# Kernel tuning notes

Measured on AMD Instinct MI355X. Metric: run time of the kernel, lower is better.

Reference implementation:

```python
import jax, jax.numpy as jnp
import numpy as np

B, N, T, H, F = 2, 1024, 12, 64, 1

def _diffuse(x, a):
    # x: (B,C,V), a: (B,W,V)  ->  (B,C,W)   (einsum 'ncvl,nwv->ncwl' with l=1)
    return jnp.einsum('bcv,bwv->bcw', x, a)

def _sconv(x, supports, order, include_self, W, b):
    feats = [x] if include_self else []
    for a in supports:
        x1 = _diffuse(x, a)
        feats.append(x1)
        for _ in range(order - 1):
            x1 = _diffuse(x1, a)
            feats.append(x1)
    z = jnp.concatenate(feats, axis=1)
    return jnp.einsum('bcn,oc->bon', z, W) + b[None, :, None]

def _lin(x, W, b):
    # Conv1d/Conv2d with kernel 1 == channel-wise linear
    return jnp.einsum('bcn,oc->bon', x, W) + b[None, :, None]

def setup_inputs():
    key = jax.random.key(0)
    ks = jax.random.split(key, 12)
    x = jax.random.normal(ks[0], (B, F, N, T), jnp.float32)
    mask = jax.random.randint(ks[1], (B, F, N, T), 0, 2, jnp.int32)
    adj = jax.random.uniform(ks[2], (2, B, N, N), jnp.float32)
    adj = adj / (adj.sum(-1, keepdims=True) + 1e-8)  # compute_support row-normalization
    cin_gate = 5 * (2 * F + H)  # (order*support_len+1)*(d_in+num_units) = 5*66
    s = 0.1
    Wr = s * jax.random.normal(ks[3], (H, cin_gate)); br = jnp.zeros((H,), jnp.float32)
    Wu = s * jax.random.normal(ks[4], (H, cin_gate)); bu = jnp.zeros((H,), jnp.float32)
    Wc = s * jax.random.normal(ks[5], (H, cin_gate)); bc = jnp.zeros((H,), jnp.float32)
    Wfs = s * jax.random.normal(ks[6], (F, H)); bfs = jnp.zeros((F,), jnp.float32)
    Wdin = s * jax.random.normal(ks[7], (H, 2 * F + H)); bdin = jnp.zeros((H,), jnp.float32)
    Wgc = s * jax.random.normal(ks[8], (H, 2 * H)); bgc = jnp.zeros((H,), jnp.float32)
    Wlout = s * jax.random.normal(ks[9], (H, 2 * H)); blout = jnp.zeros((H,), jnp.float32)
    Wro = s * jax.random.normal(ks[10], (F, 2 * H)); bro = jnp.zeros((F,), jnp.float32)
    prelu_a = 0.25 * jnp.ones((1,), jnp.float32)
    return dict(x=x, mask=mask, adj=adj, Wr=Wr, br=br, Wu=Wu, bu=bu, Wc=Wc, bc=bc,
                Wfs=Wfs, bfs=bfs, Wdin=Wdin, bdin=bdin, Wgc=Wgc, bgc=bgc,
                Wlout=Wlout, blout=blout, Wro=Wro, bro=bro, prelu_a=prelu_a)

def _gril(x, mask, adj, Wr, br, Wu, bu, Wc, bc, Wfs, bfs, Wdin, bdin,
          Wgc, bgc, Wlout, blout, Wro, bro, prelu_a):
    supports = [adj[0], adj[1]]
    h0 = jnp.zeros((x.shape[0], H, x.shape[2]), x.dtype)

    def step(h, inp):
        x_s, m_s = inp                  # (B,F,N), (B,F,N) int
        m_f = m_s.astype(x_s.dtype)
        m_b = m_s.astype(bool)
        # first stage prediction from hidden state
        xs1 = _lin(h, Wfs, bfs)
        x1 = jnp.where(m_b, x_s, xs1)
        # spatial decoder (order=1, no attention)
        x_in = _lin(jnp.concatenate([x1, m_f, h], axis=1), Wdin, bdin)
        out = _sconv(x_in, supports, 1, False, Wgc, bgc)
        out = _lin(jnp.concatenate([out, h], axis=1), Wlout, blout)
        out = jnp.where(out >= 0, out, prelu_a * out)   # PReLU
        repr_s = jnp.concatenate([out, h], axis=1)      # (B,2H,N)
        xs2 = _lin(repr_s, Wro, bro)
        x2 = jnp.where(m_b, x1, xs2)
        # GCGRU cell update (order=2 diffusion per gate)
        inp_c = jnp.concatenate([x2, m_f], axis=1)
        xh = jnp.concatenate([inp_c, h], axis=1)
        r = jax.nn.sigmoid(_sconv(xh, supports, 2, True, Wr, br))
        u = jax.nn.sigmoid(_sconv(xh, supports, 2, True, Wu, bu))
        xc = jnp.concatenate([inp_c, r * h], axis=1)
        c = jnp.tanh(_sconv(xc, supports, 2, True, Wc, bc))
        h_new = u * h + (1.0 - u) * c
        return h_new, (xs2, xs1, repr_s)

    xs = jnp.moveaxis(x, -1, 0)     # (T,B,F,N)
    ms = jnp.moveaxis(mask, -1, 0)
    _, (imps, preds, reprs) = jax.lax.scan(step, h0, (xs, ms))
    imputations = jnp.moveaxis(imps, 0, -1)       # (B,F,N,T)
    predictions = jnp.moveaxis(preds, 0, -1)      # (B,F,N,T)
    representations = jnp.moveaxis(reprs, 0, -1)  # (B,2H,N,T)
    return imputations, predictions, representations

def reference(x, mask, adj, Wr, br, Wu, bu, Wc, bc, Wfs, bfs, Wdin, bdin,
              Wgc, bgc, Wlout, blout, Wro, bro, prelu_a):
    return _gril(x, mask, adj, Wr, br, Wu, bu, Wc, bc, Wfs, bfs, Wdin, bdin,
                 Wgc, bgc, Wlout, blout, Wro, bro, prelu_a)
```

## Files before the change

kernel.cpp:

```cpp
#include <hip/hip_runtime.h>
#include <hip/hip_bf16.h>
#include <cstddef>

#define NN 1024
#define BB 2
#define TT 12
#define ZS 352

typedef __attribute__((ext_vector_type(8))) short short8;
typedef __attribute__((ext_vector_type(4))) short short4v;
typedef __attribute__((ext_vector_type(4))) float f32x4;
typedef __hip_bfloat16 bf16;

__device__ __forceinline__ float sigmoidf_(float v) { return 1.0f / (1.0f + expf(-v)); }
__device__ __forceinline__ short bf16s(float f) { bf16 h = __float2bfloat16(f); return *reinterpret_cast<short*>(&h); }

__device__ __forceinline__ float mapcol(const float* src, int c) {
    if (c < 64) return src[2 + c];
    if (c == 64) return src[0];
    if (c == 65) return src[1];
    if (c < 68 || c >= 340) return 0.f;
    const int d = c - 68, bk = d / 68, off = d % 68;
    if (off < 64) return src[66 + bk * 66 + 2 + off];
    if (off == 64) return src[66 + bk * 66];
    if (off == 65) return src[66 + bk * 66 + 1];
    return 0.f;
}

__global__ __launch_bounds__(256) void k_prep(
    const float* __restrict__ Wgc, const float* __restrict__ bgc,
    const float* __restrict__ Wdin, const float* __restrict__ bdin,
    const float* __restrict__ Wlout, const float* __restrict__ blout,
    const float* __restrict__ Wfs,
    const float* __restrict__ Wr, const float* __restrict__ Wu, const float* __restrict__ Wc,
    float* __restrict__ Wcomb, float* __restrict__ bcomb, float* __restrict__ blout2,
    bf16* __restrict__ Wpre, bf16* __restrict__ Wrub, bf16* __restrict__ Wcb,
    bf16* __restrict__ Wlb)
{
    const int idx = blockIdx.x * 256 + threadIdx.x;
    if (idx < 8448) {
        const int o = idx / 66, k = idx % 66;
        const float* g = Wgc + (size_t)(o & 63) * 128 + (o >> 6) * 64;
        float a = 0.f;
#pragma unroll 8
        for (int c = 0; c < 64; ++c) a += g[c] * Wdin[c * 66 + k];
        Wcomb[idx] = a;
    } else if (idx < 8576) {
        const int o = idx - 8448;
        const float* g = Wgc + (size_t)(o & 63) * 128 + (o >> 6) * 64;
        float a = 0.f;
#pragma unroll 8
        for (int c = 0; c < 64; ++c) a += g[c] * bdin[c];
        bcomb[o] = a;
    } else if (idx < 8640) {
        const int oc = idx - 8576;
        float a = blout[oc];
#pragma unroll 8
        for (int j = 0; j < 64; ++j) a += Wlout[(size_t)oc * 128 + j] * bgc[j];
        blout2[oc] = a;
    } else if (idx < 17856) {
        const int j = idx - 8640, r = j >> 6, k = j & 63;
        float v = 0.f;
        if (r == 0) v = Wfs[k];
        else if (r <= 128) {
            const int o = r - 1;
            const float* g = Wgc + (size_t)(o & 63) * 128 + (o >> 6) * 64;
#pragma unroll 8
            for (int c = 0; c < 64; ++c) v += g[c] * Wdin[c * 66 + 2 + k];
        }
        Wpre[j] = __float2bfloat16(v);
    } else if (idx < 62912) {
        const int j = idx - 17856, r = j / 352, c = j % 352;
        const float* src = (r < 64) ? (Wr + (size_t)r * 330) : (Wu + (size_t)(r - 64) * 330);
        Wrub[j] = __float2bfloat16(mapcol(src, c));
    } else if (idx < 85440) {
        const int j = idx - 62912, r = j / 352, c = j % 352;
        Wcb[j] = __float2bfloat16(mapcol(Wc + (size_t)r * 330, c));
    } else if (idx < 93632) {
        const int j = idx - 85440;
        Wlb[j] = __float2bfloat16(Wlout[j]);
    }
}

__global__ __launch_bounds__(256) void k_cvtT(const float* __restrict__ adj,
                                              bf16* __restrict__ adjb, bf16* __restrict__ adjtb)
{
    const int sb = blockIdx.z;
    const int r0 = blockIdx.y * 64, c0 = blockIdx.x * 64;
    const float* A = adj + ((size_t)sb << 20);
    __shared__ short tile[64][72];
    const int tr = threadIdx.x >> 4, tc = (threadIdx.x & 15) * 4;
#pragma unroll
    for (int i = 0; i < 4; ++i) {
        const int r = tr + i * 16;
        float4 v = *reinterpret_cast<const float4*>(&A[(size_t)(r0 + r) * NN + c0 + tc]);
        short4v o = { bf16s(v.x), bf16s(v.y), bf16s(v.z), bf16s(v.w) };
        *reinterpret_cast<short4v*>(&adjb[((size_t)sb << 20) + (size_t)(r0 + r) * NN + c0 + tc]) = o;
        tile[r][tc + 0] = o.x; tile[r][tc + 1] = o.y; tile[r][tc + 2] = o.z; tile[r][tc + 3] = o.w;
    }
    __syncthreads();
#pragma unroll
    for (int i = 0; i < 4; ++i) {
        const int v = tr + i * 16;
        short4v o = { tile[tc + 0][v], tile[tc + 1][v], tile[tc + 2][v], tile[tc + 3][v] };
        *reinterpret_cast<short4v*>(&adjtb[((size_t)sb << 20) + (size_t)(c0 + v) * NN + r0 + tc]) = o;
    }
}

__global__ __launch_bounds__(256) void k_a2(const bf16* __restrict__ adjb,
                                            const bf16* __restrict__ adjtb,
                                            bf16* __restrict__ adj2b)
{
    const int sb = blockIdx.z;
    const int wave = threadIdx.x >> 6, lane = threadIdx.x & 63;
    const int lr = lane & 15, lq = lane >> 4;
    const int v0 = blockIdx.x * 128 + wave * 32;
    const int w0 = blockIdx.y * 64;
    const bf16* AT = adjtb + ((size_t)sb << 20) + (size_t)(v0 + lr) * NN + lq * 8;
    const bf16* Ar = adjb + ((size_t)sb << 20) + (size_t)(w0 + lr) * NN + lq * 8;
    f32x4 acc[4][2];
#pragma unroll
    for (int m = 0; m < 4; ++m)
#pragma unroll
        for (int nb = 0; nb < 2; ++nb) acc[m][nb] = (f32x4){0.f, 0.f, 0.f, 0.f};

    short8 bfr[2], af[4];
#pragma unroll
    for (int nb = 0; nb < 2; ++nb) bfr[nb] = *reinterpret_cast<const short8*>(AT + (size_t)nb * 16 * NN);
#pragma unroll
    for (int m = 0; m < 4; ++m) af[m] = *reinterpret_cast<const short8*>(Ar + (size_t)m * 16 * NN);

#pragma unroll 4
    for (int k0 = 0; k0 < NN; k0 += 32) {
        short8 bfr_n[2], af_n[4];
        const int kn = k0 + 32;
        if (kn < NN) {
#pragma unroll
            for (int nb = 0; nb < 2; ++nb)
                bfr_n[nb] = *reinterpret_cast<const short8*>(AT + (size_t)nb * 16 * NN + kn);
#pragma unroll
            for (int m = 0; m < 4; ++m)
                af_n[m] = *reinterpret_cast<const short8*>(Ar + (size_t)m * 16 * NN + kn);
        }
#pragma unroll
        for (int m = 0; m < 4; ++m)
#pragma unroll
            for (int nb = 0; nb < 2; ++nb)
                acc[m][nb] = __builtin_amdgcn_mfma_f32_16x16x32_bf16(af[m], bfr[nb], acc[m][nb], 0, 0, 0);
        if (kn < NN) {
#pragma unroll
            for (int nb = 0; nb < 2; ++nb) bfr[nb] = bfr_n[nb];
#pragma unroll
            for (int m = 0; m < 4; ++m) af[m] = af_n[m];
        }
    }
    bf16* D = adj2b + ((size_t)sb << 20);
#pragma unroll
    for (int m = 0; m < 4; ++m)
#pragma unroll
        for (int nb = 0; nb < 2; ++nb)
#pragma unroll
            for (int q = 0; q < 4; ++q)
                D[(size_t)(w0 + m * 16 + lq * 4 + q) * NN + v0 + nb * 16 + lr] = __float2bfloat16(acc[m][nb][q]);
}

__global__ __launch_bounds__(64) void k_pre(
    const bf16* __restrict__ Wpre, const bf16* __restrict__ zT,
    const float* __restrict__ Wcomb, const float* __restrict__ bcomb,
    const float* __restrict__ bfsp,
    const float* __restrict__ x, const int* __restrict__ mask,
    bf16* __restrict__ yb, float* __restrict__ pred, int t)
{
    const int lane = threadIdx.x & 63, lr = lane & 15, lq = lane >> 4;
    const int p = blockIdx.x * 16 + lr;
    const bf16* B = zT + (size_t)p * ZS;
    f32x4 acc[9];
#pragma unroll
    for (int m = 0; m < 9; ++m) acc[m] = (f32x4){0.f, 0.f, 0.f, 0.f};
#pragma unroll
    for (int ks = 0; ks < 2; ++ks) {
        short8 bfr = *reinterpret_cast<const short8*>(B + ks * 32 + lq * 8);
#pragma unroll
        for (int m = 0; m < 9; ++m) {
            short8 af = *reinterpret_cast<const short8*>(Wpre + (size_t)(m * 16 + lr) * 64 + ks * 32 + lq * 8);
            acc[m] = __builtin_amdgcn_mfma_f32_16x16x32_bf16(af, bfr, acc[m], 0, 0, 0);
        }
    }
    const int b = p >> 10, n = p & (NN - 1);
    const size_t xi = (size_t)p * TT + t;
    const float xs1v = acc[0][0] + bfsp[0];
    const float xs1 = __shfl(xs1v, lr);
    const int mi = mask[xi];
    const float mf = (float)mi;
    const float x1 = mi ? x[xi] : xs1;
    if (lq == 0) pred[xi] = xs1;
#pragma unroll
    for (int m = 0; m < 9; ++m)
#pragma unroll
        for (int q = 0; q < 4; ++q) {
            const int o = m * 16 + lq * 4 + q - 1;
            if (o >= 0 && o < 128) {
                const float val = acc[m][q] + Wcomb[o * 66] * x1 + Wcomb[o * 66 + 1] * mf + bcomb[o];
                yb[(size_t)(b * 128 + o) * NN + n] = __float2bfloat16(val);
            }
        }
}

__global__ __launch_bounds__(256) void k_difA(
    const bf16* __restrict__ adjb, const bf16* __restrict__ adj2b,
    const bf16* __restrict__ yb, const bf16* __restrict__ zbi,
    const bf16* __restrict__ Wlb, const float* __restrict__ blout2,
    const float* __restrict__ prelu_a, const float* __restrict__ Wro,
    const float* __restrict__ bro, const float* __restrict__ x,
    const int* __restrict__ mask, const float* __restrict__ hTf,
    float* __restrict__ imp, float* __restrict__ repr,
    bf16* __restrict__ zb, bf16* __restrict__ zcb,
    bf16* __restrict__ zT, bf16* __restrict__ zcT, int t)
{
    const int wave = threadIdx.x >> 6, lane = threadIdx.x & 63;
    const int lr = lane & 15, lq = lane >> 4;
    const int n0 = blockIdx.x * 32;

    __shared__ f32x4 red[3][2][2][4][64];
    __shared__ short gh[32][136];
    __shared__ float hf[32][68];
    __shared__ float lo_sm[32][68];

    if (blockIdx.y >= 2) {
        const int i = blockIdx.y - 2;
        const int b = i & 1, s = (i >> 1) & 1, ord = i >> 2;
        const int sb = s * 2 + b;
        const bf16* M = (ord ? adj2b : adjb) + ((size_t)sb << 20);
        const bf16* A = M + (size_t)(n0 + lr) * NN + lq * 8;
        const bf16* Xp = zbi + ((size_t)(b * 66 + lr)) * NN + lq * 8;
        f32x4 acc[2][4];
#pragma unroll
        for (int nt = 0; nt < 2; ++nt)
#pragma unroll
            for (int m = 0; m < 4; ++m) acc[nt][m] = (f32x4){0.f, 0.f, 0.f, 0.f};
        const int vbeg = wave * 256;
#pragma unroll 2
        for (int it = 0; it < 8; ++it) {
            const int v0 = vbeg + it * 32;
            short8 bfr[2], af[4];
#pragma unroll
            for (int nt = 0; nt < 2; ++nt)
                bfr[nt] = *reinterpret_cast<const short8*>(A + (size_t)nt * 16 * NN + v0);
#pragma unroll
            for (int m = 0; m < 4; ++m)
                af[m] = *reinterpret_cast<const short8*>(Xp + (size_t)m * 16 * NN + v0);
#pragma unroll
            for (int nt = 0; nt < 2; ++nt)
#pragma unroll
                for (int m = 0; m < 4; ++m)
                    acc[nt][m] = __builtin_amdgcn_mfma_f32_16x16x32_bf16(af[m], bfr[nt], acc[nt][m], 0, 0, 0);
        }
        if (wave > 0) {
#pragma unroll
            for (int nt = 0; nt < 2; ++nt)
#pragma unroll
                for (int m = 0; m < 4; ++m) red[wave - 1][0][nt][m][lane] = acc[nt][m];
        }
        __syncthreads();
        if (wave == 0) {
#pragma unroll
            for (int nt = 0; nt < 2; ++nt) {
#pragma unroll
                for (int m = 0; m < 4; ++m)
                    acc[nt][m] += red[0][0][nt][m][lane] + red[1][0][nt][m][lane] + red[2][0][nt][m][lane];
                const int p = b * NN + n0 + nt * 16 + lr;
                bf16* dst = zT + (size_t)p * ZS + 68 + (s * 2 + ord) * 68;
#pragma unroll
                for (int m = 0; m < 4; ++m) {
                    short4v o = { bf16s(acc[nt][m][0]), bf16s(acc[nt][m][1]),
                                  bf16s(acc[nt][m][2]), bf16s(acc[nt][m][3]) };
                    *reinterpret_cast<short4v*>(dst + m * 16 + lq * 4) = o;
                }
            }
        }
        return;
    }

    const int b = blockIdx.y;
    f32x4 acc[2][2][4];
#pragma unroll
    for (int s = 0; s < 2; ++s)
#pragma unroll
        for (int nt = 0; nt < 2; ++nt)
#pragma unroll
            for (int m = 0; m < 4; ++m) acc[s][nt][m] = (f32x4){0.f, 0.f, 0.f, 0.f};
    {
        const int vbeg = wave * 256;
#pragma unroll 2
        for (int it = 0; it < 8; ++it) {
            const int v0 = vbeg + it * 32;
            short8 bfr[2][2], af[2][4];
#pragma unroll
            for (int s = 0; s < 2; ++s) {
                const bf16* M = adjb + ((size_t)(s * 2 + b) << 20);
#pragma unroll
                for (int nt = 0; nt < 2; ++nt)
                    bfr[s][nt] = *reinterpret_cast<const short8*>(M + (size_t)(n0 + nt * 16 + lr) * NN + v0 + lq * 8);
#pragma unroll
                for (int m = 0; m < 4; ++m)
                    af[s][m] = *reinterpret_cast<const short8*>(yb + (size_t)(b * 128 + s * 64 + m * 16 + lr) * NN + v0 + lq * 8);
            }
#pragma unroll
            for (int s = 0; s < 2; ++s)
#pragma unroll
                for (int nt = 0; nt < 2; ++nt)
#pragma unroll
                    for (int m = 0; m < 4; ++m)
                        acc[s][nt][m] = __builtin_amdgcn_mfma_f32_16x16x32_bf16(af[s][m], bfr[s][nt], acc[s][nt][m], 0, 0, 0);
        }
    }
    if (wave > 0) {
#pragma unroll
        for (int s = 0; s < 2; ++s)
#pragma unroll
            for (int nt = 0; nt < 2; ++nt)
#pragma unroll
                for (int m = 0; m < 4; ++m) red[wave - 1][s][nt][m][lane] = acc[s][nt][m];
    }
    if (wave == 1 || wave == 2) {
        const int nb = (wave - 1) * 16;
        for (int i = lane; i < 1024; i += 64) {
            const int node = nb + (i >> 6), oc = i & 63;
            const float hv = hTf[(size_t)(b * NN + n0 + node) * 64 + oc];
            hf[node][oc] = hv;
            gh[node][64 + oc] = bf16s(hv);
            repr[(((size_t)b * 128 + 64 + oc) * NN + (n0 + node)) * TT + t] = hv;
        }
    }
    __syncthreads();
    if (wave == 0) {
#pragma unroll
        for (int nt = 0; nt < 2; ++nt) {
#pragma unroll
            for (int m = 0; m < 4; ++m) {
                f32x4 g = acc[0][nt][m] + acc[1][nt][m];
#pragma unroll
                for (int w = 0; w < 3; ++w) g += red[w][0][nt][m][lane] + red[w][1][nt][m][lane];
                const int node = nt * 16 + lr;
#pragma unroll
                for (int q = 0; q < 4; ++q) gh[node][m * 16 + lq * 4 + q] = bf16s(g[q]);
            }
        }
    }
    __syncthreads();
    {
        f32x4 dacc[2];
#pragma unroll
        for (int nt = 0; nt < 2; ++nt) dacc[nt] = (f32x4){0.f, 0.f, 0.f, 0.f};
#pragma unroll
        for (int ks = 0; ks < 4; ++ks) {
            short8 af = *reinterpret_cast<const short8*>(Wlb + (size_t)(wave * 16 + lr) * 128 + ks * 32 + lq * 8);
#pragma unroll
            for (int nt = 0; nt < 2; ++nt) {
                short8 bfr = *reinterpret_cast<const short8*>(&gh[nt * 16 + lr][ks * 32 + lq * 8]);
                dacc[nt] = __builtin_amdgcn_mfma_f32_16x16x32_bf16(af, bfr, dacc[nt], 0, 0, 0);
            }
        }
        const float pa = prelu_a[0];
#pragma unroll
        for (int nt = 0; nt < 2; ++nt) {
            const int node = nt * 16 + lr;
#pragma unroll
            for (int q = 0; q < 4; ++q) {
                const int oc = wave * 16 + lq * 4 + q;
                float v = dacc[nt][q] + blout2[oc];
                v = (v >= 0.f) ? v : pa * v;
                repr[(((size_t)b * 128 + oc) * NN + (n0 + node)) * TT + t] = v;
                lo_sm[node][oc] = v;
            }
        }
    }
    __syncthreads();
    {
        const int node = threadIdx.x >> 3, sub = threadIdx.x & 7;
        float s = 0.f;
#pragma unroll
        for (int j = sub * 8; j < sub * 8 + 8; ++j)
            s += Wro[j] * lo_sm[node][j] + Wro[64 + j] * hf[node][j];
        s += __shfl_xor(s, 1); s += __shfl_xor(s, 2); s += __shfl_xor(s, 4);
        if (sub == 0) {
            const float xs2 = s + bro[0];
            const int n = n0 + node;
            const int p = b * NN + n;
            const size_t xi = (size_t)p * TT + t;
            imp[xi] = xs2;
            const int mi = mask[xi];
            const float x2 = mi ? x[xi] : xs2;
            const bf16 x2b = __float2bfloat16(x2);
            const bf16 mb = __float2bfloat16((float)mi);
            zb[((size_t)b * 66 + 64) * NN + n] = x2b;
            zb[((size_t)b * 66 + 65) * NN + n] = mb;
            zT[(size_t)p * ZS + 64] = x2b; zT[(size_t)p * ZS + 65] = mb;
            zcT[(size_t)p * ZS + 64] = x2b; zcT[(size_t)p * ZS + 65] = mb;
        }
    }
}

__global__ __launch_bounds__(256) void k_difN(
    const bf16* __restrict__ adjb, const bf16* __restrict__ adj2b,
    const bf16* __restrict__ zcb, bf16* __restrict__ zcT)
{
    const int i = blockIdx.y;
    const int b = i & 1, s = (i >> 1) & 1, ord = i >> 2;
    const int wave = threadIdx.x >> 6, lane = threadIdx.x & 63;
    const int lr = lane & 15, lq = lane >> 4;
    const int n0 = blockIdx.x * 32;
    const int sb = s * 2 + b;
    const bf16* M = (ord ? adj2b : adjb) + ((size_t)sb << 20);
    const bf16* A = M + (size_t)(n0 + lr) * NN + lq * 8;
    const bf16* Xp = zcb + ((size_t)(b * 66 + lr)) * NN + lq * 8;

    f32x4 acc[2][4];
#pragma unroll
    for (int nt = 0; nt < 2; ++nt)
#pragma unroll
        for (int m = 0; m < 4; ++m) acc[nt][m] = (f32x4){0.f, 0.f, 0.f, 0.f};
    const int vbeg = wave * 256;

    short8 bfr[2], af[4];
#pragma unroll
    for (int nt = 0; nt < 2; ++nt)
        bfr[nt] = *reinterpret_cast<const short8*>(A + (size_t)nt * 16 * NN + vbeg);
#pragma unroll
    for (int m = 0; m < 4; ++m)
        af[m] = *reinterpret_cast<const short8*>(Xp + (size_t)m * 16 * NN + vbeg);

#pragma unroll 2
    for (int it = 0; it < 8; ++it) {
        const int vn = vbeg + it * 32 + 32;
        short8 bfr_n[2], af_n[4];
        if (it < 7) {
#pragma unroll
            for (int nt = 0; nt < 2; ++nt)
                bfr_n[nt] = *reinterpret_cast<const short8*>(A + (size_t)nt * 16 * NN + vn);
#pragma unroll
            for (int m = 0; m < 4; ++m)
                af_n[m] = *reinterpret_cast<const short8*>(Xp + (size_t)m * 16 * NN + vn);
        }
#pragma unroll
        for (int nt = 0; nt < 2; ++nt)
#pragma unroll
            for (int m = 0; m < 4; ++m)
                acc[nt][m] = __builtin_amdgcn_mfma_f32_16x16x32_bf16(af[m], bfr[nt], acc[nt][m], 0, 0, 0);
        if (it < 7) {
#pragma unroll
            for (int nt = 0; nt < 2; ++nt) bfr[nt] = bfr_n[nt];
#pragma unroll
            for (int m = 0; m < 4; ++m) af[m] = af_n[m];
        }
    }
    __shared__ f32x4 red[3][2][4][64];
    if (wave > 0) {
#pragma unroll
        for (int nt = 0; nt < 2; ++nt)
#pragma unroll
            for (int m = 0; m < 4; ++m) red[wave - 1][nt][m][lane] = acc[nt][m];
    }
    __syncthreads();
    if (wave == 0) {
#pragma unroll
        for (int nt = 0; nt < 2; ++nt) {
#pragma unroll
            for (int m = 0; m < 4; ++m)
                acc[nt][m] += red[0][nt][m][lane] + red[1][nt][m][lane] + red[2][nt][m][lane];
            const int p = b * NN + n0 + nt * 16 + lr;
            bf16* dst = zcT + (size_t)p * ZS + 68 + (s * 2 + ord) * 68;
#pragma unroll
            for (int m = 0; m < 4; ++m) {
                short4v o = { bf16s(acc[nt][m][0]), bf16s(acc[nt][m][1]),
                              bf16s(acc[nt][m][2]), bf16s(acc[nt][m][3]) };
                *reinterpret_cast<short4v*>(dst + m * 16 + lq * 4) = o;
            }
        }
    }
}

__global__ __launch_bounds__(256) void k_dif2(
    const bf16* __restrict__ adjb, const bf16* __restrict__ adj2b,
    const bf16* __restrict__ zb, bf16* __restrict__ zT, bf16* __restrict__ zcT)
{
    const int i = blockIdx.y;
    const int b = i & 1, s = (i >> 1) & 1, ord = i >> 2;
    const int sb = s * 2 + b;
    const int wave = threadIdx.x >> 6, lane = threadIdx.x & 63;
    const int lr = lane & 15, lq = lane >> 4;
    const int n0 = blockIdx.x * 16;
    const bf16* M = (ord ? adj2b : adjb) + ((size_t)sb << 20);
    const bf16* A = M + (size_t)(n0 + lr) * NN + lq * 8;
    const bf16* Xp = zb + ((size_t)(b * 66 + 64) + lr) * NN + lq * 8;

    f32x4 acc = (f32x4){0.f, 0.f, 0.f, 0.f};
    const short8 zsh = {0, 0, 0, 0, 0, 0, 0, 0};
    const int vbeg = wave * 256;
#pragma unroll 4
    for (int i2 = 0; i2 < 8; ++i2) {
        const int v0 = vbeg + i2 * 32;
        short8 bfr = *reinterpret_cast<const short8*>(A + v0);
        short8 af = (lr < 2) ? *reinterpret_cast<const short8*>(Xp + v0) : zsh;
        acc = __builtin_amdgcn_mfma_f32_16x16x32_bf16(af, bfr, acc, 0, 0, 0);
    }
    __shared__ f32x4 red2[3][64];
    if (wave > 0) red2[wave - 1][lane] = acc;
    __syncthreads();
    if (wave == 0 && lq == 0) {
        acc += red2[0][lane] + red2[1][lane] + red2[2][lane];
        const int p = b * NN + n0 + lr;
        const size_t off = (size_t)p * ZS + 68 + (s * 2 + ord) * 68 + 64;
#pragma unroll
        for (int q = 0; q < 2; ++q) {
            const bf16 v = __float2bfloat16(acc[q]);
            zT[off + q] = v; zcT[off + q] = v;
        }
    }
}

__global__ __launch_bounds__(128) void k_gates(
    const bf16* __restrict__ Wrub, const bf16* __restrict__ zT,
    const float* __restrict__ br, const float* __restrict__ bu,
    const float* __restrict__ hTf,
    float* __restrict__ uT, bf16* __restrict__ zcb, bf16* __restrict__ zcT)
{
    const int wave = threadIdx.x >> 6, lane = threadIdx.x & 63;
    const int lr = lane & 15, lq = lane >> 4;
    const int p = blockIdx.x * 16 + lr;
    const bf16* B = zT + (size_t)p * ZS;
    const bf16* WA = Wrub + (size_t)wave * 64 * ZS;
    f32x4 acc[4];
#pragma unroll
    for (int m = 0; m < 4; ++m) acc[m] = (f32x4){0.f, 0.f, 0.f, 0.f};
#pragma unroll 2
    for (int ks = 0; ks < 11; ++ks) {
        short8 bfr = *reinterpret_cast<const short8*>(B + ks * 32 + lq * 8);
#pragma unroll
        for (int m = 0; m < 4; ++m) {
            short8 af = *reinterpret_cast<const short8*>(WA + (size_t)(m * 16 + lr) * ZS + ks * 32 + lq * 8);
            acc[m] = __builtin_amdgcn_mfma_f32_16x16x32_bf16(af, bfr, acc[m], 0, 0, 0);
        }
    }
    const int b = p >> 10, n = p & (NN - 1);
    if (wave == 0) {
#pragma unroll
        for (int m = 0; m < 4; ++m) {
            short4v rq;
#pragma unroll
            for (int q = 0; q < 4; ++q) {
                const int oc = m * 16 + lq * 4 + q;
                const float rv = sigmoidf_(acc[m][q] + br[oc]);
                const float rh = rv * hTf[(size_t)p * 64 + oc];
                rq[q] = bf16s(rh);
                zcb[((size_t)b * 66 + oc) * NN + n] = __float2bfloat16(rh);
            }
            *reinterpret_cast<short4v*>(&zcT[(size_t)p * ZS + m * 16 + lq * 4]) = rq;
        }
    } else {
#pragma unroll
        for (int m = 0; m < 4; ++m) {
            f32x4 uq;
#pragma unroll
            for (int q = 0; q < 4; ++q) {
                const int oc = m * 16 + lq * 4 + q;
                uq[q] = sigmoidf_(acc[m][q] + bu[oc]);
            }
            *reinterpret_cast<f32x4*>(&uT[(size_t)p * 64 + m * 16 + lq * 4]) = uq;
        }
    }
}

__global__ __launch_bounds__(128) void k_cellpre(
    const bf16* __restrict__ Wcb, const bf16* __restrict__ zcT,
    const float* __restrict__ bc, const float* __restrict__ uT,
    float* __restrict__ hTf, bf16* __restrict__ zT, bf16* __restrict__ zb,
    const bf16* __restrict__ Wpre, const float* __restrict__ Wcomb,
    const float* __restrict__ bcomb, const float* __restrict__ bfsp,
    const float* __restrict__ x, const int* __restrict__ mask,
    bf16* __restrict__ yb, float* __restrict__ pred, int tn)
{
    const int wave = threadIdx.x >> 6, lane = threadIdx.x & 63;
    const int lr = lane & 15, lq = lane >> 4;
    const int p = blockIdx.x * 16 + lr;
    const int b = p >> 10, n = p & (NN - 1);
    __shared__ short hsm[16][72];
    __shared__ float xs1s[16];

    {
        const bf16* B = zcT + (size_t)p * ZS;
        f32x4 acc[2];
#pragma unroll
        for (int mm = 0; mm < 2; ++mm) acc[mm] = (f32x4){0.f, 0.f, 0.f, 0.f};
#pragma unroll 2
        for (int ks = 0; ks < 11; ++ks) {
            short8 bfr = *reinterpret_cast<const short8*>(B + ks * 32 + lq * 8);
#pragma unroll
            for (int mm = 0; mm < 2; ++mm) {
                const int m = wave * 2 + mm;
                short8 af = *reinterpret_cast<const short8*>(Wcb + (size_t)(m * 16 + lr) * ZS + ks * 32 + lq * 8);
                acc[mm] = __builtin_amdgcn_mfma_f32_16x16x32_bf16(af, bfr, acc[mm], 0, 0, 0);
            }
        }
#pragma unroll
        for (int mm = 0; mm < 2; ++mm) {
            const int m = wave * 2 + mm;
            f32x4 hq;
            short4v hb;
#pragma unroll
            for (int q = 0; q < 4; ++q) {
                const int oc = m * 16 + lq * 4 + q;
                const float cv = tanhf(acc[mm][q] + bc[oc]);
                const float uv = uT[(size_t)p * 64 + oc];
                const float ho = hTf[(size_t)p * 64 + oc];
                const float hn = uv * ho + (1.f - uv) * cv;
                hq[q] = hn;
                hb[q] = bf16s(hn);
                zb[((size_t)b * 66 + oc) * NN + n] = __float2bfloat16(hn);
            }
            *reinterpret_cast<f32x4*>(&hTf[(size_t)p * 64 + m * 16 + lq * 4]) = hq;
            *reinterpret_cast<short4v*>(&zT[(size_t)p * ZS + m * 16 + lq * 4]) = hb;
            *reinterpret_cast<short4v*>(&hsm[lr][m * 16 + lq * 4]) = hb;
        }
    }
    __syncthreads();

    {
        const int MB = wave ? 4 : 5;
        f32x4 acc[5];
#pragma unroll
        for (int m = 0; m < 5; ++m) acc[m] = (f32x4){0.f, 0.f, 0.f, 0.f};
#pragma unroll
        for (int ks = 0; ks < 2; ++ks) {
            short8 bfr = *reinterpret_cast<const short8*>(&hsm[lr][ks * 32 + lq * 8]);
#pragma unroll
            for (int m = 0; m < 5; ++m) {
                if (m < MB) {
                    const int mm = wave ? 5 + m : m;
                    short8 af = *reinterpret_cast<const short8*>(Wpre + (size_t)(mm * 16 + lr) * 64 + ks * 32 + lq * 8);
                    acc[m] = __builtin_amdgcn_mfma_f32_16x16x32_bf16(af, bfr, acc[m], 0, 0, 0);
                }
            }
        }
        if (wave == 0 && lq == 0) xs1s[lr] = acc[0][0] + bfsp[0];
        __syncthreads();
        const float xs1 = xs1s[lr];
        const size_t xi = (size_t)p * TT + tn;
        const int mi = mask[xi];
        const float mf = (float)mi;
        const float x1 = mi ? x[xi] : xs1;
        if (wave == 0 && lq == 0) pred[xi] = xs1;
#pragma unroll
        for (int m = 0; m < 5; ++m) {
            if (m < MB) {
                const int mm = wave ? 5 + m : m;
#pragma unroll
                for (int q = 0; q < 4; ++q) {
                    const int o = mm * 16 + lq * 4 + q - 1;
                    if (o >= 0 && o < 128) {
                        const float val = acc[m][q] + Wcomb[o * 66] * x1 + Wcomb[o * 66 + 1] * mf + bcomb[o];
                        yb[(size_t)(b * 128 + o) * NN + n] = __float2bfloat16(val);
                    }
                }
            }
        }
    }
}

extern "C" void kernel_launch(void* const* d_in, const int* in_sizes, int n_in,
                              void* d_out, int out_size, void* d_ws, size_t ws_size,
                              hipStream_t stream)
{
    const float* x     = (const float*)d_in[0];
    const int*   mask  = (const int*)  d_in[1];
    const float* adj   = (const float*)d_in[2];
    const float* Wr    = (const float*)d_in[3];
    const float* br    = (const float*)d_in[4];
    const float* Wu    = (const float*)d_in[5];
    const float* bu    = (const float*)d_in[6];
    const float* Wc    = (const float*)d_in[7];
    const float* bc    = (const float*)d_in[8];
    const float* Wfs   = (const float*)d_in[9];
    const float* bfs   = (const float*)d_in[10];
    const float* Wdin  = (const float*)d_in[11];
    const float* bdin  = (const float*)d_in[12];
    const float* Wgc   = (const float*)d_in[13];
    const float* bgc   = (const float*)d_in[14];
    const float* Wlout = (const float*)d_in[15];
    const float* blout = (const float*)d_in[16];
    const float* Wro   = (const float*)d_in[17];
    const float* bro   = (const float*)d_in[18];
    const float* pa    = (const float*)d_in[19];

    float* ws = (float*)d_ws;
    float* Wcomb  = ws + 0;
    float* bcomb  = ws + 8448;
    float* blout2 = ws + 8576;
    float* uT     = ws + 272832;
    float* hTf    = ws + 403904;
    bf16* bfp   = (bf16*)(ws + 534976);
    bf16* zb    = bfp + 0;
    bf16* zcb   = bfp + 135168;
    bf16* zT    = bfp + 270336;
    bf16* zcT   = bfp + 991232;
    bf16* adjb  = bfp + 1712128;
    bf16* adjtb = bfp + 5906432;
    bf16* adj2b = bfp + 10100736;
    bf16* yb    = bfp + 14295040;
    bf16* Wpre  = bfp + 14557184;
    bf16* Wrub  = bfp + 14566400;
    bf16* Wcb   = bfp + 14611456;
    bf16* Wlb   = bfp + 14633984;

    float* imp  = (float*)d_out;
    float* pred = imp + (size_t)BB * NN * TT;
    float* repr = imp + (size_t)2 * BB * NN * TT;

    hipMemsetAsync(hTf, 0, 131072 * 4 + (size_t)1712128 * 2, stream);
    hipLaunchKernelGGL(k_prep, dim3(366), dim3(256), 0, stream,
                       Wgc, bgc, Wdin, bdin, Wlout, blout, Wfs, Wr, Wu, Wc,
                       Wcomb, bcomb, blout2, Wpre, Wrub, Wcb, Wlb);
    hipLaunchKernelGGL(k_cvtT, dim3(16, 16, 4), dim3(256), 0, stream, adj, adjb, adjtb);
    hipLaunchKernelGGL(k_a2, dim3(8, 16, 4), dim3(256), 0, stream, adjb, adjtb, adj2b);

    hipLaunchKernelGGL(k_pre, dim3(128), dim3(64), 0, stream,
                       Wpre, zT, Wcomb, bcomb, bfs, x, mask, yb, pred, 0);

    for (int t = 0; t < TT; ++t) {
        const int ny = (t > 0 && t < TT - 1) ? 10 : 2;
        hipLaunchKernelGGL(k_difA, dim3(32, ny), dim3(256), 0, stream,
                           adjb, adj2b, yb, zb, Wlb, blout2, pa, Wro, bro, x, mask,
                           hTf, imp, repr, zb, zcb, zT, zcT, t);
        if (t < TT - 1) {
            hipLaunchKernelGGL(k_dif2, dim3(64, 8), dim3(256), 0, stream,
                               adjb, adj2b, zb, zT, zcT);
            hipLaunchKernelGGL(k_gates, dim3(128), dim3(128), 0, stream,
                               Wrub, zT, br, bu, hTf, uT, zcb, zcT);
            if (t > 0) {
                hipLaunchKernelGGL(k_difN, dim3(32, 8), dim3(256), 0, stream,
                                   adjb, adj2b, zcb, zcT);
            }
            hipLaunchKernelGGL(k_cellpre, dim3(128), dim3(128), 0, stream,
                               Wcb, zcT, bc, uT, hTf, zT, zb,
                               Wpre, Wcomb, bcomb, bfs, x, mask, yb, pred, t + 1);
        }
    }
}
```

Baseline: 695.5 us.

## Fuse mask-channel diffusion into gates kernel with rank-8 correction

```diff
diff --git a/kernel.cpp b/kernel.cpp
--- a/kernel.cpp
+++ b/kernel.cpp
@@ -26,6 +26,15 @@
     if (off == 65) return src[66 + bk * 66 + 1];
     return 0.f;
 }
+__device__ __forceinline__ float mapcolz(const float* src, int c) {
+    if (c < 64) return src[2 + c];
+    if (c == 64) return src[0];
+    if (c == 65) return src[1];
+    if (c < 68 || c >= 340) return 0.f;
+    const int d = c - 68, bk = d / 68, off = d % 68;
+    if (off < 64) return src[66 + bk * 66 + 2 + off];
+    return 0.f;
+}
 
 __global__ __launch_bounds__(256) void k_prep(
     const float* __restrict__ Wgc, const float* __restrict__ bgc,
@@ -35,7 +44,7 @@
     const float* __restrict__ Wr, const float* __restrict__ Wu, const float* __restrict__ Wc,
     float* __restrict__ Wcomb, float* __restrict__ bcomb, float* __restrict__ blout2,
     bf16* __restrict__ Wpre, bf16* __restrict__ Wrub, bf16* __restrict__ Wcb,
-    bf16* __restrict__ Wlb)
+    bf16* __restrict__ Wlb, float* __restrict__ Wrux)
 {
     const int idx = blockIdx.x * 256 + threadIdx.x;
     if (idx < 8448) {
@@ -72,13 +81,17 @@
     } else if (idx < 62912) {
         const int j = idx - 17856, r = j / 352, c = j % 352;
         const float* src = (r < 64) ? (Wr + (size_t)r * 330) : (Wu + (size_t)(r - 64) * 330);
-        Wrub[j] = __float2bfloat16(mapcol(src, c));
+        Wrub[j] = __float2bfloat16(mapcolz(src, c));
     } else if (idx < 85440) {
         const int j = idx - 62912, r = j / 352, c = j % 352;
         Wcb[j] = __float2bfloat16(mapcol(Wc + (size_t)r * 330, c));
     } else if (idx < 93632) {
         const int j = idx - 85440;
         Wlb[j] = __float2bfloat16(Wlout[j]);
+    } else if (idx < 94656) {
+        const int j2 = idx - 93632, r = j2 >> 3, j = j2 & 7;
+        const float* src = (r < 64) ? (Wr + (size_t)r * 330) : (Wu + (size_t)(r - 64) * 330);
+        Wrux[j2] = src[66 + (j >> 1) * 66 + (j & 1)];
     }
 }
 
@@ -111,11 +124,14 @@
                                             const bf16* __restrict__ adjtb,
                                             bf16* __restrict__ adj2b)
 {
-    const int sb = blockIdx.z;
+    const int L = blockIdx.x;
+    const int xv = L >> 6;
+    const int yz = L & 63;
+    const int w0 = (yz & 15) * 64;
+    const int sb = yz >> 4;
     const int wave = threadIdx.x >> 6, lane = threadIdx.x & 63;
     const int lr = lane & 15, lq = lane >> 4;
-    const int v0 = blockIdx.x * 128 + wave * 32;
-    const int w0 = blockIdx.y * 64;
+    const int v0 = xv * 128 + wave * 32;
     const bf16* AT = adjtb + ((size_t)sb << 20) + (size_t)(v0 + lr) * NN + lq * 8;
     const bf16* Ar = adjb + ((size_t)sb << 20) + (size_t)(w0 + lr) * NN + lq * 8;
     f32x4 acc[4][2];
@@ -123,36 +139,20 @@
     for (int m = 0; m < 4; ++m)
 #pragma unroll
         for (int nb = 0; nb < 2; ++nb) acc[m][nb] = (f32x4){0.f, 0.f, 0.f, 0.f};
-
-    short8 bfr[2], af[4];
-#pragma unroll
-    for (int nb = 0; nb < 2; ++nb) bfr[nb] = *reinterpret_cast<const short8*>(AT + (size_t)nb * 16 * NN);
-#pragma unroll
-    for (int m = 0; m < 4; ++m) af[m] = *reinterpret_cast<const short8*>(Ar + (size_t)m * 16 * NN);
-
 #pragma unroll 4
     for (int k0 = 0; k0 < NN; k0 += 32) {
-        short8 bfr_n[2], af_n[4];
-        const int kn = k0 + 32;
-        if (kn < NN) {
-#pragma unroll
-            for (int nb = 0; nb < 2; ++nb)
-                bfr_n[nb] = *reinterpret_cast<const short8*>(AT + (size_t)nb * 16 * NN + kn);
-#pragma unroll
-            for (int m = 0; m < 4; ++m)
-                af_n[m] = *reinterpret_cast<const short8*>(Ar + (size_t)m * 16 * NN + kn);
-        }
+        short8 bfr[2], af[4];
+#pragma unroll
+        for (int nb = 0; nb < 2; ++nb)
+            bfr[nb] = *reinterpret_cast<const short8*>(AT + (size_t)nb * 16 * NN + k0);
+#pragma unroll
+        for (int m = 0; m < 4; ++m)
+            af[m] = *reinterpret_cast<const short8*>(Ar + (size_t)m * 16 * NN + k0);
 #pragma unroll
         for (int m = 0; m < 4; ++m)
 #pragma unroll
             for (int nb = 0; nb < 2; ++nb)
                 acc[m][nb] = __builtin_amdgcn_mfma_f32_16x16x32_bf16(af[m], bfr[nb], acc[m][nb], 0, 0, 0);
-        if (kn < NN) {
-#pragma unroll
-            for (int nb = 0; nb < 2; ++nb) bfr[nb] = bfr_n[nb];
-#pragma unroll
-            for (int m = 0; m < 4; ++m) af[m] = af_n[m];
-        }
     }
     bf16* D = adj2b + ((size_t)sb << 20);
 #pragma unroll
@@ -480,93 +480,103 @@
     }
 }
 
-__global__ __launch_bounds__(256) void k_dif2(
-    const bf16* __restrict__ adjb, const bf16* __restrict__ adj2b,
-    const bf16* __restrict__ zb, bf16* __restrict__ zT, bf16* __restrict__ zcT)
-{
-    const int i = blockIdx.y;
-    const int b = i & 1, s = (i >> 1) & 1, ord = i >> 2;
-    const int sb = s * 2 + b;
-    const int wave = threadIdx.x >> 6, lane = threadIdx.x & 63;
-    const int lr = lane & 15, lq = lane >> 4;
-    const int n0 = blockIdx.x * 16;
-    const bf16* M = (ord ? adj2b : adjb) + ((size_t)sb << 20);
-    const bf16* A = M + (size_t)(n0 + lr) * NN + lq * 8;
-    const bf16* Xp = zb + ((size_t)(b * 66 + 64) + lr) * NN + lq * 8;
-
-    f32x4 acc = (f32x4){0.f, 0.f, 0.f, 0.f};
-    const short8 zsh = {0, 0, 0, 0, 0, 0, 0, 0};
-    const int vbeg = wave * 256;
-#pragma unroll 4
-    for (int i2 = 0; i2 < 8; ++i2) {
-        const int v0 = vbeg + i2 * 32;
-        short8 bfr = *reinterpret_cast<const short8*>(A + v0);
-        short8 af = (lr < 2) ? *reinterpret_cast<const short8*>(Xp + v0) : zsh;
-        acc = __builtin_amdgcn_mfma_f32_16x16x32_bf16(af, bfr, acc, 0, 0, 0);
-    }
-    __shared__ f32x4 red2[3][64];
-    if (wave > 0) red2[wave - 1][lane] = acc;
-    __syncthreads();
-    if (wave == 0 && lq == 0) {
-        acc += red2[0][lane] + red2[1][lane] + red2[2][lane];
-        const int p = b * NN + n0 + lr;
-        const size_t off = (size_t)p * ZS + 68 + (s * 2 + ord) * 68 + 64;
-#pragma unroll
-        for (int q = 0; q < 2; ++q) {
-            const bf16 v = __float2bfloat16(acc[q]);
-            zT[off + q] = v; zcT[off + q] = v;
-        }
-    }
-}
-
-__global__ __launch_bounds__(128) void k_gates(
+__global__ __launch_bounds__(512) void k_gates(
     const bf16* __restrict__ Wrub, const bf16* __restrict__ zT,
     const float* __restrict__ br, const float* __restrict__ bu,
     const float* __restrict__ hTf,
+    const bf16* __restrict__ adjb, const bf16* __restrict__ adj2b,
+    const bf16* __restrict__ zb, const float* __restrict__ Wrux,
     float* __restrict__ uT, bf16* __restrict__ zcb, bf16* __restrict__ zcT)
 {
     const int wave = threadIdx.x >> 6, lane = threadIdx.x & 63;
     const int lr = lane & 15, lq = lane >> 4;
     const int p = blockIdx.x * 16 + lr;
-    const bf16* B = zT + (size_t)p * ZS;
-    const bf16* WA = Wrub + (size_t)wave * 64 * ZS;
-    f32x4 acc[4];
-#pragma unroll
-    for (int m = 0; m < 4; ++m) acc[m] = (f32x4){0.f, 0.f, 0.f, 0.f};
+    const int b = blockIdx.x >> 6;
+    const int n0 = (blockIdx.x & 63) * 16;
+    const int n = p & (NN - 1);
+    __shared__ float xds[8][16];
+    __shared__ float wxs[128][8];
+
+    f32x4 acc[2];
+    acc[0] = (f32x4){0.f, 0.f, 0.f, 0.f};
+    acc[1] = (f32x4){0.f, 0.f, 0.f, 0.f};
+
+    if (wave < 4) {
+        const int ti = wave * 64 + lane;
+        reinterpret_cast<float4*>(&wxs[0][0])[ti] = reinterpret_cast<const float4*>(Wrux)[ti];
+        const bf16* B = zT + (size_t)p * ZS;
 #pragma unroll 2
-    for (int ks = 0; ks < 11; ++ks) {
-        short8 bfr = *reinterpret_cast<const short8*>(B + ks * 32 + lq * 8);
-#pragma unroll
-        for (int m = 0; m < 4; ++m) {
-            short8 af = *reinterpret_cast<const short8*>(WA + (size_t)(m * 16 + lr) * ZS + ks * 32 + lq * 8);
-            acc[m] = __builtin_amdgcn_mfma_f32_16x16x32_bf16(af, bfr, acc[m], 0, 0, 0);
-        }
-    }
-    const int b = p >> 10, n = p & (NN - 1);
-    if (wave == 0) {
-#pragma unroll
-        for (int m = 0; m < 4; ++m) {
-            short4v rq;
-#pragma unroll
-            for (int q = 0; q < 4; ++q) {
-                const int oc = m * 16 + lq * 4 + q;
-                const float rv = sigmoidf_(acc[m][q] + br[oc]);
-                const float rh = rv * hTf[(size_t)p * 64 + oc];
-                rq[q] = bf16s(rh);
-                zcb[((size_t)b * 66 + oc) * NN + n] = __float2bfloat16(rh);
-            }
-            *reinterpret_cast<short4v*>(&zcT[(size_t)p * ZS + m * 16 + lq * 4]) = rq;
+        for (int ks = 0; ks < 11; ++ks) {
+            short8 bfr = *reinterpret_cast<const short8*>(B + ks * 32 + lq * 8);
+#pragma unroll
+            for (int mm = 0; mm < 2; ++mm) {
+                short8 af = *reinterpret_cast<const short8*>(
+                    Wrub + (size_t)(wave * 32 + mm * 16 + lr) * ZS + ks * 32 + lq * 8);
+                acc[mm] = __builtin_amdgcn_mfma_f32_16x16x32_bf16(af, bfr, acc[mm], 0, 0, 0);
+            }
         }
     } else {
-#pragma unroll
-        for (int m = 0; m < 4; ++m) {
-            f32x4 uq;
-#pragma unroll
-            for (int q = 0; q < 4; ++q) {
-                const int oc = m * 16 + lq * 4 + q;
-                uq[q] = sigmoidf_(acc[m][q] + bu[oc]);
-            }
-            *reinterpret_cast<f32x4*>(&uT[(size_t)p * 64 + m * 16 + lq * 4]) = uq;
+        const int bk = wave - 4;
+        const int s = bk >> 1, ord = bk & 1;
+        const bf16* Mp = (ord ? adj2b : adjb) + ((size_t)(s * 2 + b) << 20)
+                         + (size_t)(n0 + lr) * NN + lq * 8;
+        const bf16* Xp = zb + (size_t)(b * 66 + 64 + lr) * NN + lq * 8;
+        const short8 zsh = {0, 0, 0, 0, 0, 0, 0, 0};
+        f32x4 a = (f32x4){0.f, 0.f, 0.f, 0.f};
+        short8 afv = (lr < 2) ? *reinterpret_cast<const short8*>(Xp) : zsh;
+        short8 mv = *reinterpret_cast<const short8*>(Mp);
+#pragma unroll 4
+        for (int it = 0; it < 32; ++it) {
+            short8 af_n, m_n;
+            if (it < 31) {
+                af_n = (lr < 2) ? *reinterpret_cast<const short8*>(Xp + (it + 1) * 32) : zsh;
+                m_n = *reinterpret_cast<const short8*>(Mp + (it + 1) * 32);
+            }
+            a = __builtin_amdgcn_mfma_f32_16x16x32_bf16(afv, mv, a, 0, 0, 0);
+            if (it < 31) { afv = af_n; mv = m_n; }
+        }
+        if (lq == 0) {
+            xds[bk * 2 + 0][lr] = a[0];
+            xds[bk * 2 + 1][lr] = a[1];
+            bf16* dst = zcT + (size_t)p * ZS + 68 + bk * 68 + 64;
+            dst[0] = __float2bfloat16(a[0]);
+            dst[1] = __float2bfloat16(a[1]);
+        }
+    }
+    __syncthreads();
+
+    if (wave < 4) {
+        if (wave < 2) {
+#pragma unroll
+            for (int mm = 0; mm < 2; ++mm) {
+                short4v rq;
+#pragma unroll
+                for (int q = 0; q < 4; ++q) {
+                    const int oc = wave * 32 + mm * 16 + lq * 4 + q;
+                    float corr = 0.f;
+#pragma unroll
+                    for (int j = 0; j < 8; ++j) corr += wxs[oc][j] * xds[j][lr];
+                    const float rv = sigmoidf_(acc[mm][q] + corr + br[oc]);
+                    const float rh = rv * hTf[(size_t)p * 64 + oc];
+                    rq[q] = bf16s(rh);
+                    zcb[((size_t)b * 66 + oc) * NN + n] = __float2bfloat16(rh);
+                }
+                *reinterpret_cast<short4v*>(&zcT[(size_t)p * ZS + (wave * 32 + mm * 16) + lq * 4]) = rq;
+            }
+        } else {
+#pragma unroll
+            for (int mm = 0; mm < 2; ++mm) {
+                f32x4 uq;
+#pragma unroll
+                for (int q = 0; q < 4; ++q) {
+                    const int ocu = (wave - 2) * 32 + mm * 16 + lq * 4 + q;
+                    float corr = 0.f;
+#pragma unroll
+                    for (int j = 0; j < 8; ++j) corr += wxs[64 + ocu][j] * xds[j][lr];
+                    uq[q] = sigmoidf_(acc[mm][q] + corr + bu[ocu]);
+                }
+                *reinterpret_cast<f32x4*>(&uT[(size_t)p * 64 + (wave - 2) * 32 + mm * 16 + lq * 4]) = uq;
+            }
         }
     }
 }
@@ -696,6 +706,7 @@
     float* Wcomb  = ws + 0;
     float* bcomb  = ws + 8448;
     float* blout2 = ws + 8576;
+    float* Wrux   = ws + 8640;
     float* uT     = ws + 272832;
     float* hTf    = ws + 403904;
     bf16* bfp   = (bf16*)(ws + 534976);
@@ -717,11 +728,11 @@
     float* repr = imp + (size_t)2 * BB * NN * TT;
 
     hipMemsetAsync(hTf, 0, 131072 * 4 + (size_t)1712128 * 2, stream);
-    hipLaunchKernelGGL(k_prep, dim3(366), dim3(256), 0, stream,
+    hipLaunchKernelGGL(k_prep, dim3(370), dim3(256), 0, stream,
                        Wgc, bgc, Wdin, bdin, Wlout, blout, Wfs, Wr, Wu, Wc,
-                       Wcomb, bcomb, blout2, Wpre, Wrub, Wcb, Wlb);
+                       Wcomb, bcomb, blout2, Wpre, Wrub, Wcb, Wlb, Wrux);
     hipLaunchKernelGGL(k_cvtT, dim3(16, 16, 4), dim3(256), 0, stream, adj, adjb, adjtb);
-    hipLaunchKernelGGL(k_a2, dim3(8, 16, 4), dim3(256), 0, stream, adjb, adjtb, adj2b);
+    hipLaunchKernelGGL(k_a2, dim3(512), dim3(256), 0, stream, adjb, adjtb, adj2b);
 
     hipLaunchKernelGGL(k_pre, dim3(128), dim3(64), 0, stream,
                        Wpre, zT, Wcomb, bcomb, bfs, x, mask, yb, pred, 0);
@@ -732,10 +743,9 @@
                            adjb, adj2b, yb, zb, Wlb, blout2, pa, Wro, bro, x, mask,
                            hTf, imp, repr, zb, zcb, zT, zcT, t);
         if (t < TT - 1) {
-            hipLaunchKernelGGL(k_dif2, dim3(64, 8), dim3(256), 0, stream,
-                               adjb, adj2b, zb, zT, zcT);
-            hipLaunchKernelGGL(k_gates, dim3(128), dim3(128), 0, stream,
-                               Wrub, zT, br, bu, hTf, uT, zcb, zcT);
+            hipLaunchKernelGGL(k_gates, dim3(128), dim3(512), 0, stream,
+                               Wrub, zT, br, bu, hTf, adjb, adj2b, zb, Wrux,
+                               uT, zcb, zcT);
             if (t > 0) {
                 hipLaunchKernelGGL(k_difN, dim3(32, 8), dim3(256), 0, stream,
                                    adjb, adj2b, zcb, zcT);
```

New measurement: 674.4 us. 3.0% less time.
